# Kernel tuning notes

Measured on AMD Instinct MI355X. Metric: run time of the kernel, lower is better.

The kernel has to match this reference:

```python
import jax, jax.numpy as jnp
import numpy as np

INPUT_CHANNELS = 1
FIRE_RATE = 0.5
BN_EPS = 1e-5
PAD = 3  # (kernel_size - 1) // 2 for kernel_size=7


def setup_inputs() -> dict:
    key = jax.random.key(0)
    ks = jax.random.split(key, 6)
    B, H, W, C, HID, K = 8, 256, 256, 16, 128, 7
    return {
        "x": jax.random.normal(ks[0], (B, H, W, C), jnp.float32),
        "p0_w": jax.random.normal(ks[1], (K, K, 1, C), jnp.float32) * 0.1,
        "p0_b": jax.random.normal(ks[2], (C,), jnp.float32) * 0.1,
        "fc0_w": jax.random.normal(ks[3], (2 * C, HID), jnp.float32) * (1.0 / np.sqrt(2 * C)),
        "fc0_b": jax.random.normal(ks[4], (HID,), jnp.float32) * 0.1,
        "bn_gamma": jnp.ones((HID,), jnp.float32),
        "bn_beta": jnp.zeros((HID,), jnp.float32),
        "fc1_w": jax.random.normal(ks[5], (HID, C), jnp.float32) * (1.0 / np.sqrt(HID)),
        "steps": 10,
    }


def _depthwise_conv(x, w, b):
    # x: [B,H,W,C], w: [K,K,1,C] depthwise, reflect padding
    xp = jnp.pad(x, ((0, 0), (PAD, PAD), (PAD, PAD), (0, 0)), mode="reflect")
    y = jax.lax.conv_general_dilated(
        xp, w, window_strides=(1, 1), padding="VALID",
        dimension_numbers=("NHWC", "HWIO", "NHWC"),
        feature_group_count=x.shape[-1])
    return y + b


def _step(x, key, p0_w, p0_b, fc0_w, fc0_b, bn_gamma, bn_beta, fc1_w):
    B, H, W, C = x.shape
    # perceive: depthwise conv + identity concat -> [B,H,W,2C]
    y = jnp.concatenate([x, _depthwise_conv(x, p0_w, p0_b)], axis=-1)
    h = y @ fc0_w + fc0_b  # [B,H,W,HID]
    # BatchNorm2d with batch stats over (N, spatial), per hidden channel
    mean = jnp.mean(h, axis=(0, 1, 2), keepdims=True)
    var = jnp.var(h, axis=(0, 1, 2), keepdims=True)
    h = (h - mean) * jax.lax.rsqrt(var + BN_EPS) * bn_gamma + bn_beta
    h = jax.nn.relu(h)
    dx = h @ fc1_w  # [B,H,W,C]
    # stochastic per-cell mask: rand > fire_rate
    mask = (jax.random.uniform(key, (B, H, W, 1)) > FIRE_RATE).astype(dx.dtype)
    x2 = x + dx * mask
    # keep input channels unchanged
    return jnp.concatenate([x[..., :INPUT_CHANNELS], x2[..., INPUT_CHANNELS:]], axis=-1)


def reference(x, p0_w, p0_b, fc0_w, fc0_b, bn_gamma, bn_beta, fc1_w, steps):
    key = jax.random.key(42)
    for s in range(steps):
        x = _step(x, jax.random.fold_in(key, s), p0_w, p0_b, fc0_w, fc0_b,
                  bn_gamma, bn_beta, fc1_w)
    return x
```

## Files before the change

kernel.cpp:

```cpp
#include <hip/hip_runtime.h>
#include <stdint.h>


constexpr int Bn = 8;
constexpr int Hn = 256;
constexpr int Wn = 256;
constexpr int Cn = 16;
constexpr int HIDn = 128;
constexpr int NCELLS = Bn * Hn * Wn;
constexpr int NGRP = 1024;
constexpr int NPAIR = 528;
constexpr int NSTAT = 560;
constexpr int STEPS = 10;
constexpr int RCELLS = 134;

typedef __attribute__((ext_vector_type(8))) short bf16x8;
typedef __attribute__((ext_vector_type(4))) float f32x4;
typedef __attribute__((ext_vector_type(2))) float f32x2;

__host__ __device__ inline uint32_t rotl32(uint32_t v, int r) {
  return (v << r) | (v >> (32 - r));
}

__host__ __device__ inline void tf2x32(uint32_t k0, uint32_t k1,
                                       uint32_t& x0, uint32_t& x1) {
  uint32_t k2 = k0 ^ k1 ^ 0x1BD11BDAu;
  x0 += k0; x1 += k1;
  x0 += x1; x1 = rotl32(x1, 13); x1 ^= x0;
  x0 += x1; x1 = rotl32(x1, 15); x1 ^= x0;
  x0 += x1; x1 = rotl32(x1, 26); x1 ^= x0;
  x0 += x1; x1 = rotl32(x1,  6); x1 ^= x0;
  x0 += k1; x1 += k2 + 1u;
  x0 += x1; x1 = rotl32(x1, 17); x1 ^= x0;
  x0 += x1; x1 = rotl32(x1, 29); x1 ^= x0;
  x0 += x1; x1 = rotl32(x1, 16); x1 ^= x0;
  x0 += x1; x1 = rotl32(x1, 24); x1 ^= x0;
  x0 += k2; x1 += k0 + 2u;
  x0 += x1; x1 = rotl32(x1, 13); x1 ^= x0;
  x0 += x1; x1 = rotl32(x1, 15); x1 ^= x0;
  x0 += x1; x1 = rotl32(x1, 26); x1 ^= x0;
  x0 += x1; x1 = rotl32(x1,  6); x1 ^= x0;
  x0 += k0; x1 += k1 + 3u;
  x0 += x1; x1 = rotl32(x1, 17); x1 ^= x0;
  x0 += x1; x1 = rotl32(x1, 29); x1 ^= x0;
  x0 += x1; x1 = rotl32(x1, 16); x1 ^= x0;
  x0 += x1; x1 = rotl32(x1, 24); x1 ^= x0;
  x0 += k1; x1 += k2 + 4u;
  x0 += x1; x1 = rotl32(x1, 13); x1 ^= x0;
  x0 += x1; x1 = rotl32(x1, 15); x1 ^= x0;
  x0 += x1; x1 = rotl32(x1, 26); x1 ^= x0;
  x0 += x1; x1 = rotl32(x1,  6); x1 ^= x0;
  x0 += k2; x1 += k0 + 5u;
}

__device__ inline float cell_mask(uint32_t fk0, uint32_t fk1, uint32_t ci) {
  uint32_t a = 0u, b2 = ci;
  tf2x32(fk0, fk1, a, b2);
  uint32_t bits = a ^ b2;
  float u = __uint_as_float((bits >> 9) | 0x3f800000u) - 1.0f;
  return (u > 0.5f) ? 1.0f : 0.0f;
}

__device__ inline uint32_t f2bf(float f) {
  uint32_t u = __float_as_uint(f);
  return (u + 0x7fffu + ((u >> 16) & 1u)) >> 16;
}

__global__ __launch_bounds__(256) void nca_prep(const float* __restrict__ fc0w,
                                                const float* __restrict__ fc1w,
                                                uint16_t* __restrict__ w0bf,
                                                uint16_t* __restrict__ w1p) {
  int i = blockIdx.x * 256 + threadIdx.x;
  if (i < 4096) {
    int n = i >> 5, k = i & 31;
    w0bf[i] = (uint16_t)f2bf(fc0w[k * HIDn + n]);
  } else {
    int j = i - 4096;
    int c = j >> 7, kl = j & 127;
    int n = (kl & 7) * 16 + (kl >> 3);
    w1p[j] = (uint16_t)f2bf(fc1w[n * 16 + c]);
  }
}

__device__ inline int row_fi(int c, int q) {
  return (((c << 6) + (q << 4)) ^ ((c & 7) << 4)) >> 2;
}

__global__ __launch_bounds__(256, 4) void nca_convgram(
    const float* __restrict__ x, const float* __restrict__ p0w,
    const float* __restrict__ p0b, uint16_t* __restrict__ ybf,
    float* __restrict__ partials) {
  __shared__ float sW[784];
  __shared__ float sB[16];
  __shared__ __align__(16) float sRow[2][RCELLS * 16];
  __shared__ __align__(16) short sYT[32 * 256];
  __shared__ float sMom[4 * 32];
  int t = threadIdx.x;
  int lane = t & 63, wid = t >> 6;
  int bid = blockIdx.x;
  int b = bid & 7;
  int rest = bid >> 3;
  int h0 = (rest >> 1) * 4;
  int wbase = (rest & 1) * 128;
  for (int i = t; i < 784; i += 256) sW[i] = p0w[i];
  if (t < 16) sB[t] = p0b[t];

  int wl = t & 127;
  int half = t >> 7;
  int ch0 = half * 8;
  int w = wbase + wl;
  const float* xb = x + (size_t)b * (Hn * Wn * Cn);

  auto rowptr = [&](int r) -> const float* {
    int hi = h0 - 3 + r;
    hi = (hi < 0) ? -hi : ((hi >= Hn) ? (2 * Hn - 2 - hi) : hi);
    return xb + (size_t)hi * (Wn * Cn);
  };
  auto ld16 = [&](const float* xr, int i) -> float4 {
    int c = i >> 2, q = i & 3;
    int wc = wbase - 3 + c;
    wc = (wc < 0) ? -wc : ((wc >= Wn) ? (2 * Wn - 2 - wc) : wc);
    return *reinterpret_cast<const float4*>(xr + (size_t)wc * Cn + q * 4);
  };

  {
    const float* xr = rowptr(0);
    float4 p0 = ld16(xr, t);
    float4 p1 = ld16(xr, t + 256);
    float4 p2;
    if (t < 536 - 512) p2 = ld16(xr, t + 512);
    float* rb = sRow[0];
    *reinterpret_cast<float4*>(rb + row_fi(t >> 2, t & 3)) = p0;
    *reinterpret_cast<float4*>(rb + row_fi((t + 256) >> 2, t & 3)) = p1;
    if (t < 536 - 512)
      *reinterpret_cast<float4*>(rb + row_fi((t + 512) >> 2, t & 3)) = p2;
  }
  __syncthreads();

  f32x2 acc2[4][4];
#pragma unroll
  for (int j = 0; j < 4; j++)
#pragma unroll
    for (int c = 0; c < 4; c++) acc2[j][c] = (f32x2){0.0f, 0.0f};

#pragma unroll 1
  for (int r = 0; r < 10; r++) {
    int cur = r & 1;
    float4 p0, p1, p2;
    if (r < 9) {
      const float* xr = rowptr(r + 1);
      p0 = ld16(xr, t);
      p1 = ld16(xr, t + 256);
      if (t < 536 - 512) p2 = ld16(xr, t + 512);
    }
    const float* rb = sRow[cur];
#pragma unroll
    for (int dx = 0; dx < 7; dx++) {
      int c = wl + dx;
      float4 va = *reinterpret_cast<const float4*>(rb + row_fi(c, 2 * half));
      float4 vb = *reinterpret_cast<const float4*>(rb + row_fi(c, 2 * half + 1));
      f32x2 v2[4];
      v2[0] = (f32x2){va.x, va.y}; v2[1] = (f32x2){va.z, va.w};
      v2[2] = (f32x2){vb.x, vb.y}; v2[3] = (f32x2){vb.z, vb.w};
#pragma unroll
      for (int j = 0; j < 4; j++) {
        if (r >= j && r <= j + 6) {
          const f32x2* wt2 = reinterpret_cast<const f32x2*>(
              sW + ((r - j) * 7 + dx) * 16 + ch0);
#pragma unroll
          for (int c2 = 0; c2 < 4; c2++) acc2[j][c2] += wt2[c2] * v2[c2];
        }
      }
    }
    if (r < 9) {
      float* wb2 = sRow[cur ^ 1];
      *reinterpret_cast<float4*>(wb2 + row_fi(t >> 2, t & 3)) = p0;
      *reinterpret_cast<float4*>(wb2 + row_fi((t + 256) >> 2, t & 3)) = p1;
      if (t < 536 - 512)
        *reinterpret_cast<float4*>(wb2 + row_fi((t + 512) >> 2, t & 3)) = p2;
    }
    __syncthreads();
  }

  int colc = lane & 15, kg = lane >> 4;
  f32x4 g00 = {0.f, 0.f, 0.f, 0.f}, g01 = g00, g11 = g00, m0 = g00, m1 = g00;
  bf16x8 ones;
#pragma unroll
  for (int e = 0; e < 8; e++) ones[e] = (short)0x3F80;

#pragma unroll
  for (int rr = 0; rr < 2; rr++) {
    if (rr) __syncthreads();
#pragma unroll
    for (int jj = 0; jj < 2; jj++) {
      int j = rr * 2 + jj;
      size_t ci = ((size_t)(b * Hn + h0 + j) * Wn + w);
      int cidx = jj * 128 + wl;
      const float4* pc = reinterpret_cast<const float4*>(
          xb + ((size_t)(h0 + j) * Wn + w) * Cn + ch0);
      float4 c0v = pc[0], c1v = pc[1];
      float xcv[8];
      xcv[0] = c0v.x; xcv[1] = c0v.y; xcv[2] = c0v.z; xcv[3] = c0v.w;
      xcv[4] = c1v.x; xcv[5] = c1v.y; xcv[6] = c1v.z; xcv[7] = c1v.w;
      uint32_t pkx[4], pkc[4];
#pragma unroll
      for (int q = 0; q < 4; q++)
        pkx[q] = f2bf(xcv[2 * q]) | (f2bf(xcv[2 * q + 1]) << 16);
#pragma unroll
      for (int q = 0; q < 4; q++)
        pkc[q] = f2bf(acc2[j][q].x + sB[ch0 + 2 * q]) |
                 (f2bf(acc2[j][q].y + sB[ch0 + 2 * q + 1]) << 16);
      *reinterpret_cast<uint4*>(ybf + ci * 32 + ch0) =
          make_uint4(pkx[0], pkx[1], pkx[2], pkx[3]);
      *reinterpret_cast<uint4*>(ybf + ci * 32 + 16 + ch0) =
          make_uint4(pkc[0], pkc[1], pkc[2], pkc[3]);
#pragma unroll
      for (int q = 0; q < 4; q++) {
        int cA = ch0 + 2 * q, cB = cA + 1;
        sYT[cA * 256 + (cidx ^ ((cA & 7) << 3))] = (short)(uint16_t)(pkx[q] & 0xffffu);
        sYT[cB * 256 + (cidx ^ ((cB & 7) << 3))] = (short)(uint16_t)(pkx[q] >> 16);
        int cC = 16 + cA, cD = 16 + cB;
        sYT[cC * 256 + (cidx ^ ((cC & 7) << 3))] = (short)(uint16_t)(pkc[q] & 0xffffu);
        sYT[cD * 256 + (cidx ^ ((cD & 7) << 3))] = (short)(uint16_t)(pkc[q] >> 16);
      }
    }
    __syncthreads();
#pragma unroll
    for (int s2 = 0; s2 < 2; s2++) {
      int kbase = wid * 64 + s2 * 32 + kg * 8;
      int chA = colc, chB = 16 + colc;
      bf16x8 f0 = *reinterpret_cast<const bf16x8*>(sYT + chA * 256 + (kbase ^ ((chA & 7) << 3)));
      bf16x8 f1 = *reinterpret_cast<const bf16x8*>(sYT + chB * 256 + (kbase ^ ((chB & 7) << 3)));
      g00 = __builtin_amdgcn_mfma_f32_16x16x32_bf16(f0, f0, g00, 0, 0, 0);
      g01 = __builtin_amdgcn_mfma_f32_16x16x32_bf16(f0, f1, g01, 0, 0, 0);
      g11 = __builtin_amdgcn_mfma_f32_16x16x32_bf16(f1, f1, g11, 0, 0, 0);
      m0  = __builtin_amdgcn_mfma_f32_16x16x32_bf16(f0, ones, m0, 0, 0, 0);
      m1  = __builtin_amdgcn_mfma_f32_16x16x32_bf16(f1, ones, m1, 0, 0, 0);
    }
  }
  if (colc == 0) {
#pragma unroll
    for (int r = 0; r < 4; r++) {
      sMom[wid * 32 + kg * 4 + r] = m0[r];
      sMom[wid * 32 + 16 + kg * 4 + r] = m1[r];
    }
  }
  __syncthreads();
  float* sG = reinterpret_cast<float*>(sYT);
  {
    float* sGw = sG + wid * 1024;
#pragma unroll
    for (int r = 0; r < 4; r++) {
      int rr2 = kg * 4 + r;
      sGw[rr2 * 32 + colc] = g00[r];
      sGw[rr2 * 32 + 16 + colc] = g01[r];
      sGw[(16 + rr2) * 32 + 16 + colc] = g11[r];
    }
  }
  __syncthreads();

  float* outp = partials + (size_t)bid * NSTAT;
  for (int e = t; e < NSTAT; e += 256) {
    float a;
    if (e < NPAIR) {
      int ee = e, i = 0;
      while (ee >= (32 - i)) { ee -= (32 - i); i++; }
      int j = i + ee;
      int gi = i * 32 + j;
      a = sG[gi] + sG[1024 + gi] + sG[2048 + gi] + sG[3072 + gi];
    } else {
      int i = e - NPAIR;
      a = sMom[i] + sMom[32 + i] + sMom[64 + i] + sMom[96 + i];
    }
    outp[e] = a;
  }
}

__global__ __launch_bounds__(256) void nca_reduceA(
    const float* __restrict__ partials, double* __restrict__ sred) {
  __shared__ double red[256][4];
  int e4 = blockIdx.x * 4;
  int t = threadIdx.x;
  double a0 = 0.0, a1 = 0.0, a2 = 0.0, a3 = 0.0;
  for (int row = t; row < NGRP; row += 256) {
    float4 v = *reinterpret_cast<const float4*>(partials + (size_t)row * NSTAT + e4);
    a0 += v.x; a1 += v.y; a2 += v.z; a3 += v.w;
  }
  red[t][0] = a0; red[t][1] = a1; red[t][2] = a2; red[t][3] = a3;
  __syncthreads();
  for (int s2 = 128; s2 > 0; s2 >>= 1) {
    if (t < s2) {
#pragma unroll
      for (int q = 0; q < 4; q++) red[t][q] += red[t + s2][q];
    }
    __syncthreads();
  }
  if (t < 4) sred[e4 + t] = red[0][t];
}

__global__ __launch_bounds__(128) void nca_reduceB(
    const double* __restrict__ sred, const float* __restrict__ fc0w,
    const float* __restrict__ gamma, const float* __restrict__ beta,
    float* __restrict__ ss) {
  __shared__ double S[NSTAT];
  int t = threadIdx.x;
  for (int i = t; i < NSTAT; i += 128) S[i] = sred[i];
  __syncthreads();
  double wv[32];
#pragma unroll
  for (int k = 0; k < 32; k++) wv[k] = (double)fc0w[k * HIDn + t];
  double mean_g = 0.0, q = 0.0;
  int e = 0;
  for (int i = 0; i < 32; i++) {
    mean_g += wv[i] * S[NPAIR + i];
    q += wv[i] * wv[i] * S[e]; e++;
    for (int j = i + 1; j < 32; j++) { q += 2.0 * wv[i] * wv[j] * S[e]; e++; }
  }
  const double invN = 1.0 / (double)NCELLS;
  mean_g *= invN; q *= invN;
  double var = q - mean_g * mean_g;
  double scale = (double)gamma[t] / sqrt(var + 1e-5);
  ss[2 * t]     = (float)scale;
  ss[2 * t + 1] = (float)((double)beta[t] - mean_g * scale);
}

__global__ __launch_bounds__(256) void nca_update_mfma(
    const float* __restrict__ x, const uint16_t* __restrict__ ybf,
    const uint16_t* __restrict__ w0bf, const uint16_t* __restrict__ w1p,
    const float* __restrict__ ssg, float* __restrict__ xout,
    uint32_t fk0, uint32_t fk1) {
  __shared__ short hbuf[4][16 * 128];
  int t = threadIdx.x;
  int lane = t & 63, wid = t >> 6;
  int col = lane & 15, g = lane >> 4;
  short* hb = hbuf[wid];

  bf16x8 b0[8];
#pragma unroll
  for (int nt = 0; nt < 8; nt++) {
    int n = nt * 16 + col;
    b0[nt] = *reinterpret_cast<const bf16x8*>(w0bf + n * 32 + g * 8);
  }
  bf16x8 b2[4];
#pragma unroll
  for (int kk = 0; kk < 4; kk++)
    b2[kk] = *reinterpret_cast<const bf16x8*>(w1p + col * 128 + kk * 32 + g * 8);
  float sc[8], sh[8];
#pragma unroll
  for (int nt = 0; nt < 8; nt++) {
    float2 v = reinterpret_cast<const float2*>(ssg)[nt * 16 + col];
    sc[nt] = v.x; sh[nt] = v.y;
  }

  uint32_t waveBase = (uint32_t)blockIdx.x * 512u + (uint32_t)wid * 128u;
  for (int grp = 0; grp < 2; grp++) {
    uint32_t grpBase = waveBase + (uint32_t)grp * 64u;
    float mval = cell_mask(fk0, fk1, grpBase + (uint32_t)lane);
#pragma unroll 1
    for (int tt = 0; tt < 4; tt++) {
      uint32_t tb = grpBase + (uint32_t)tt * 16u;
      bf16x8 a0 = *reinterpret_cast<const bf16x8*>(
          ybf + (size_t)(tb + col) * 32 + g * 8);
      float xv[4];
#pragma unroll
      for (int r = 0; r < 4; r++)
        xv[r] = x[(size_t)(tb + g * 4 + r) * Cn + col];
      f32x4 h[8];
#pragma unroll
      for (int nt = 0; nt < 8; nt++) {
        f32x4 z = {0.f, 0.f, 0.f, 0.f};
        h[nt] = __builtin_amdgcn_mfma_f32_16x16x32_bf16(a0, b0[nt], z, 0, 0, 0);
      }
#pragma unroll
      for (int r = 0; r < 4; r++) {
        int m = g * 4 + r;
        uint32_t u[4];
#pragma unroll
        for (int q = 0; q < 4; q++) {
          float v0 = fmaxf(h[2 * q][r] * sc[2 * q] + sh[2 * q], 0.0f);
          float v1 = fmaxf(h[2 * q + 1][r] * sc[2 * q + 1] + sh[2 * q + 1], 0.0f);
          u[q] = f2bf(v0) | (f2bf(v1) << 16);
        }
        int idx = m * 128 + ((col * 8) ^ ((m & 7) << 3));
        *reinterpret_cast<uint4*>(hb + idx) = make_uint4(u[0], u[1], u[2], u[3]);
      }
      f32x4 dx = {0.f, 0.f, 0.f, 0.f};
#pragma unroll
      for (int kk = 0; kk < 4; kk++) {
        int idx = col * 128 + (((kk * 32) + g * 8) ^ ((col & 7) << 3));
        bf16x8 a2 = *reinterpret_cast<const bf16x8*>(hb + idx);
        dx = __builtin_amdgcn_mfma_f32_16x16x32_bf16(a2, b2[kk], dx, 0, 0, 0);
      }
#pragma unroll
      for (int r = 0; r < 4; r++) {
        int m = g * 4 + r;
        float mk = __shfl(mval, tt * 16 + m);
        float o = xv[r] + dx[r] * mk;
        if (col == 0) o = xv[r];
        xout[(size_t)(tb + m) * Cn + col] = o;
      }
    }
  }
}

extern "C" void kernel_launch(void* const* d_in, const int* in_sizes, int n_in,
                              void* d_out, int out_size, void* d_ws, size_t ws_size,
                              hipStream_t stream) {
  (void)in_sizes; (void)n_in; (void)out_size; (void)ws_size;
  const float* x0    = (const float*)d_in[0];
  const float* p0w   = (const float*)d_in[1];
  const float* p0b   = (const float*)d_in[2];
  const float* fc0w  = (const float*)d_in[3];
  const float* gamma = (const float*)d_in[5];
  const float* beta  = (const float*)d_in[6];
  const float* fc1w  = (const float*)d_in[7];

  size_t off = 0;
  float* ws_x = (float*)((char*)d_ws + off); off += (size_t)NCELLS * Cn * 4;
  uint16_t* ws_ybf = (uint16_t*)((char*)d_ws + off); off += (size_t)NCELLS * 32 * 2;
  float* ws_part = (float*)((char*)d_ws + off); off += (size_t)NGRP * NSTAT * 4;
  double* ws_sred = (double*)((char*)d_ws + off); off += (size_t)NSTAT * 8;
  float* ws_ss = (float*)((char*)d_ws + off); off += (size_t)HIDn * 2 * 4;
  uint16_t* ws_w0bf = (uint16_t*)((char*)d_ws + off); off += 4096 * 2;
  uint16_t* ws_w1p = (uint16_t*)((char*)d_ws + off); off += 2048 * 2;
  float* out = (float*)d_out;

  nca_prep<<<24, 256, 0, stream>>>(fc0w, fc1w, ws_w0bf, ws_w1p);

  const float* xin = x0;
  for (int s = 0; s < STEPS; s++) {
    uint32_t fk0 = 0u, fk1 = (uint32_t)s;
    tf2x32(0u, 42u, fk0, fk1);
    float* xo = (((STEPS - 1 - s) & 1) != 0) ? ws_x : out;

    nca_convgram<<<NGRP, 256, 0, stream>>>(xin, p0w, p0b, ws_ybf, ws_part);
    nca_reduceA<<<140, 256, 0, stream>>>(ws_part, ws_sred);
    nca_reduceB<<<1, 128, 0, stream>>>(ws_sred, fc0w, gamma, beta, ws_ss);
    nca_update_mfma<<<NCELLS / 512, 256, 0, stream>>>(xin, ws_ybf, ws_w0bf,
                                                      ws_w1p, ws_ss, xo, fk0, fk1);
    xin = xo;
  }
}
```

Measured before the change: 752.7 us.

## Halve conv-gram tile width and alias row buffer with transpose scratch in LDS

The conv+Gram kernel now processes 64-wide column tiles with each thread owning 4 channels instead of 8, doubling the number of blocks (NGRP 1024→2048). The row double-buffer and the bf16 transpose buffer now share one 16KB LDS region, and the Gram MFMA phase runs once over all 4 rows instead of two half passes. The intent is lower LDS and register use per block for higher occupancy, plus fewer barriers. In exchange the halo overhead per cell grows (70 loaded cells for 64 outputs), and twice as many partial-stat blocks must be reduced.

```diff
diff --git a/kernel.cpp b/kernel.cpp
--- a/kernel.cpp
+++ b/kernel.cpp
@@ -8,11 +8,12 @@
 constexpr int Cn = 16;
 constexpr int HIDn = 128;
 constexpr int NCELLS = Bn * Hn * Wn;
-constexpr int NGRP = 1024;
+constexpr int NGRP = 2048;
 constexpr int NPAIR = 528;
 constexpr int NSTAT = 560;
 constexpr int STEPS = 10;
-constexpr int RCELLS = 134;
+constexpr int RCELLS = 70;
+constexpr int RUNITS = RCELLS * 4;
 
 typedef __attribute__((ext_vector_type(8))) short bf16x8;
 typedef __attribute__((ext_vector_type(4))) float f32x4;
@@ -92,22 +93,23 @@
     float* __restrict__ partials) {
   __shared__ float sW[784];
   __shared__ float sB[16];
-  __shared__ __align__(16) float sRow[2][RCELLS * 16];
-  __shared__ __align__(16) short sYT[32 * 256];
+  __shared__ __align__(16) char uMem[16384];
   __shared__ float sMom[4 * 32];
+  float* sRowBuf = reinterpret_cast<float*>(uMem);
+  short* sYT = reinterpret_cast<short*>(uMem);
   int t = threadIdx.x;
   int lane = t & 63, wid = t >> 6;
   int bid = blockIdx.x;
   int b = bid & 7;
   int rest = bid >> 3;
-  int h0 = (rest >> 1) * 4;
-  int wbase = (rest & 1) * 128;
+  int h0 = (rest >> 2) * 4;
+  int wbase = (rest & 3) * 64;
   for (int i = t; i < 784; i += 256) sW[i] = p0w[i];
   if (t < 16) sB[t] = p0b[t];
 
-  int wl = t & 127;
-  int half = t >> 7;
-  int ch0 = half * 8;
+  int wl = t & 63;
+  int chq = t >> 6;
+  int ch0 = chq * 4;
   int w = wbase + wl;
   const float* xb = x + (size_t)b * (Hn * Wn * Cn);
 
@@ -126,117 +128,100 @@
   {
     const float* xr = rowptr(0);
     float4 p0 = ld16(xr, t);
-    float4 p1 = ld16(xr, t + 256);
-    float4 p2;
-    if (t < 536 - 512) p2 = ld16(xr, t + 512);
-    float* rb = sRow[0];
+    float4 p1;
+    if (t < RUNITS - 256) p1 = ld16(xr, t + 256);
+    float* rb = sRowBuf;
     *reinterpret_cast<float4*>(rb + row_fi(t >> 2, t & 3)) = p0;
-    *reinterpret_cast<float4*>(rb + row_fi((t + 256) >> 2, t & 3)) = p1;
-    if (t < 536 - 512)
-      *reinterpret_cast<float4*>(rb + row_fi((t + 512) >> 2, t & 3)) = p2;
-  }
-  __syncthreads();
-
-  f32x2 acc2[4][4];
-#pragma unroll
-  for (int j = 0; j < 4; j++)
-#pragma unroll
-    for (int c = 0; c < 4; c++) acc2[j][c] = (f32x2){0.0f, 0.0f};
+    if (t < RUNITS - 256)
+      *reinterpret_cast<float4*>(rb + row_fi((t >> 2) + 64, t & 3)) = p1;
+  }
+  __syncthreads();
+
+  f32x2 acc2[4][2];
+#pragma unroll
+  for (int j = 0; j < 4; j++) {
+    acc2[j][0] = (f32x2){0.0f, 0.0f};
+    acc2[j][1] = (f32x2){0.0f, 0.0f};
+  }
 
 #pragma unroll 1
   for (int r = 0; r < 10; r++) {
     int cur = r & 1;
-    float4 p0, p1, p2;
+    float4 p0, p1;
     if (r < 9) {
       const float* xr = rowptr(r + 1);
       p0 = ld16(xr, t);
-      p1 = ld16(xr, t + 256);
-      if (t < 536 - 512) p2 = ld16(xr, t + 512);
-    }
-    const float* rb = sRow[cur];
+      if (t < RUNITS - 256) p1 = ld16(xr, t + 256);
+    }
+    const float* rb = sRowBuf + cur * (RCELLS * 16);
 #pragma unroll
     for (int dx = 0; dx < 7; dx++) {
       int c = wl + dx;
-      float4 va = *reinterpret_cast<const float4*>(rb + row_fi(c, 2 * half));
-      float4 vb = *reinterpret_cast<const float4*>(rb + row_fi(c, 2 * half + 1));
-      f32x2 v2[4];
-      v2[0] = (f32x2){va.x, va.y}; v2[1] = (f32x2){va.z, va.w};
-      v2[2] = (f32x2){vb.x, vb.y}; v2[3] = (f32x2){vb.z, vb.w};
+      float4 va = *reinterpret_cast<const float4*>(rb + row_fi(c, chq));
+      f32x2 v0 = (f32x2){va.x, va.y};
+      f32x2 v1 = (f32x2){va.z, va.w};
 #pragma unroll
       for (int j = 0; j < 4; j++) {
         if (r >= j && r <= j + 6) {
           const f32x2* wt2 = reinterpret_cast<const f32x2*>(
               sW + ((r - j) * 7 + dx) * 16 + ch0);
-#pragma unroll
-          for (int c2 = 0; c2 < 4; c2++) acc2[j][c2] += wt2[c2] * v2[c2];
+          acc2[j][0] += wt2[0] * v0;
+          acc2[j][1] += wt2[1] * v1;
         }
       }
     }
     if (r < 9) {
-      float* wb2 = sRow[cur ^ 1];
+      float* wb2 = sRowBuf + (cur ^ 1) * (RCELLS * 16);
       *reinterpret_cast<float4*>(wb2 + row_fi(t >> 2, t & 3)) = p0;
-      *reinterpret_cast<float4*>(wb2 + row_fi((t + 256) >> 2, t & 3)) = p1;
-      if (t < 536 - 512)
-        *reinterpret_cast<float4*>(wb2 + row_fi((t + 512) >> 2, t & 3)) = p2;
+      if (t < RUNITS - 256)
+        *reinterpret_cast<float4*>(wb2 + row_fi((t >> 2) + 64, t & 3)) = p1;
     }
     __syncthreads();
   }
+
+#pragma unroll
+  for (int j = 0; j < 4; j++) {
+    size_t ci = ((size_t)(b * Hn + h0 + j) * Wn + w);
+    int cidx = j * 64 + wl;
+    float4 cv = *reinterpret_cast<const float4*>(
+        xb + ((size_t)(h0 + j) * Wn + w) * Cn + ch0);
+    uint32_t pkx[2], pkc[2];
+    pkx[0] = f2bf(cv.x) | (f2bf(cv.y) << 16);
+    pkx[1] = f2bf(cv.z) | (f2bf(cv.w) << 16);
+    pkc[0] = f2bf(acc2[j][0].x + sB[ch0 + 0]) |
+             (f2bf(acc2[j][0].y + sB[ch0 + 1]) << 16);
+    pkc[1] = f2bf(acc2[j][1].x + sB[ch0 + 2]) |
+             (f2bf(acc2[j][1].y + sB[ch0 + 3]) << 16);
+    *reinterpret_cast<uint2*>(ybf + ci * 32 + ch0) = make_uint2(pkx[0], pkx[1]);
+    *reinterpret_cast<uint2*>(ybf + ci * 32 + 16 + ch0) = make_uint2(pkc[0], pkc[1]);
+#pragma unroll
+    for (int q = 0; q < 2; q++) {
+      int cA = ch0 + 2 * q, cB = cA + 1;
+      sYT[cA * 256 + (cidx ^ ((cA & 7) << 3))] = (short)(uint16_t)(pkx[q] & 0xffffu);
+      sYT[cB * 256 + (cidx ^ ((cB & 7) << 3))] = (short)(uint16_t)(pkx[q] >> 16);
+      int cC = 16 + cA, cD = 16 + cB;
+      sYT[cC * 256 + (cidx ^ ((cC & 7) << 3))] = (short)(uint16_t)(pkc[q] & 0xffffu);
+      sYT[cD * 256 + (cidx ^ ((cD & 7) << 3))] = (short)(uint16_t)(pkc[q] >> 16);
+    }
+  }
+  __syncthreads();
 
   int colc = lane & 15, kg = lane >> 4;
   f32x4 g00 = {0.f, 0.f, 0.f, 0.f}, g01 = g00, g11 = g00, m0 = g00, m1 = g00;
   bf16x8 ones;
 #pragma unroll
   for (int e = 0; e < 8; e++) ones[e] = (short)0x3F80;
-
-#pragma unroll
-  for (int rr = 0; rr < 2; rr++) {
-    if (rr) __syncthreads();
-#pragma unroll
-    for (int jj = 0; jj < 2; jj++) {
-      int j = rr * 2 + jj;
-      size_t ci = ((size_t)(b * Hn + h0 + j) * Wn + w);
-      int cidx = jj * 128 + wl;
-      const float4* pc = reinterpret_cast<const float4*>(
-          xb + ((size_t)(h0 + j) * Wn + w) * Cn + ch0);
-      float4 c0v = pc[0], c1v = pc[1];
-      float xcv[8];
-      xcv[0] = c0v.x; xcv[1] = c0v.y; xcv[2] = c0v.z; xcv[3] = c0v.w;
-      xcv[4] = c1v.x; xcv[5] = c1v.y; xcv[6] = c1v.z; xcv[7] = c1v.w;
-      uint32_t pkx[4], pkc[4];
-#pragma unroll
-      for (int q = 0; q < 4; q++)
-        pkx[q] = f2bf(xcv[2 * q]) | (f2bf(xcv[2 * q + 1]) << 16);
-#pragma unroll
-      for (int q = 0; q < 4; q++)
-        pkc[q] = f2bf(acc2[j][q].x + sB[ch0 + 2 * q]) |
-                 (f2bf(acc2[j][q].y + sB[ch0 + 2 * q + 1]) << 16);
-      *reinterpret_cast<uint4*>(ybf + ci * 32 + ch0) =
-          make_uint4(pkx[0], pkx[1], pkx[2], pkx[3]);
-      *reinterpret_cast<uint4*>(ybf + ci * 32 + 16 + ch0) =
-          make_uint4(pkc[0], pkc[1], pkc[2], pkc[3]);
-#pragma unroll
-      for (int q = 0; q < 4; q++) {
-        int cA = ch0 + 2 * q, cB = cA + 1;
-        sYT[cA * 256 + (cidx ^ ((cA & 7) << 3))] = (short)(uint16_t)(pkx[q] & 0xffffu);
-        sYT[cB * 256 + (cidx ^ ((cB & 7) << 3))] = (short)(uint16_t)(pkx[q] >> 16);
-        int cC = 16 + cA, cD = 16 + cB;
-        sYT[cC * 256 + (cidx ^ ((cC & 7) << 3))] = (short)(uint16_t)(pkc[q] & 0xffffu);
-        sYT[cD * 256 + (cidx ^ ((cD & 7) << 3))] = (short)(uint16_t)(pkc[q] >> 16);
-      }
-    }
-    __syncthreads();
-#pragma unroll
-    for (int s2 = 0; s2 < 2; s2++) {
-      int kbase = wid * 64 + s2 * 32 + kg * 8;
-      int chA = colc, chB = 16 + colc;
-      bf16x8 f0 = *reinterpret_cast<const bf16x8*>(sYT + chA * 256 + (kbase ^ ((chA & 7) << 3)));
-      bf16x8 f1 = *reinterpret_cast<const bf16x8*>(sYT + chB * 256 + (kbase ^ ((chB & 7) << 3)));
-      g00 = __builtin_amdgcn_mfma_f32_16x16x32_bf16(f0, f0, g00, 0, 0, 0);
-      g01 = __builtin_amdgcn_mfma_f32_16x16x32_bf16(f0, f1, g01, 0, 0, 0);
-      g11 = __builtin_amdgcn_mfma_f32_16x16x32_bf16(f1, f1, g11, 0, 0, 0);
-      m0  = __builtin_amdgcn_mfma_f32_16x16x32_bf16(f0, ones, m0, 0, 0, 0);
-      m1  = __builtin_amdgcn_mfma_f32_16x16x32_bf16(f1, ones, m1, 0, 0, 0);
-    }
+#pragma unroll
+  for (int s2 = 0; s2 < 2; s2++) {
+    int kbase = wid * 64 + s2 * 32 + kg * 8;
+    int chA = colc, chB = 16 + colc;
+    bf16x8 f0 = *reinterpret_cast<const bf16x8*>(sYT + chA * 256 + (kbase ^ ((chA & 7) << 3)));
+    bf16x8 f1 = *reinterpret_cast<const bf16x8*>(sYT + chB * 256 + (kbase ^ ((chB & 7) << 3)));
+    g00 = __builtin_amdgcn_mfma_f32_16x16x32_bf16(f0, f0, g00, 0, 0, 0);
+    g01 = __builtin_amdgcn_mfma_f32_16x16x32_bf16(f0, f1, g01, 0, 0, 0);
+    g11 = __builtin_amdgcn_mfma_f32_16x16x32_bf16(f1, f1, g11, 0, 0, 0);
+    m0  = __builtin_amdgcn_mfma_f32_16x16x32_bf16(f0, ones, m0, 0, 0, 0);
+    m1  = __builtin_amdgcn_mfma_f32_16x16x32_bf16(f1, ones, m1, 0, 0, 0);
   }
   if (colc == 0) {
 #pragma unroll
@@ -246,7 +231,7 @@
     }
   }
   __syncthreads();
-  float* sG = reinterpret_cast<float*>(sYT);
+  float* sG = reinterpret_cast<float*>(uMem);
   {
     float* sGw = sG + wid * 1024;
 #pragma unroll
```

After: 1.342 ms. 1.78x slower.
